# Kernel optimization log

Hardware: AMD Instinct MI355X
Metric: run time of the kernel (lower is better)

Reference implementation:

```python
import jax, jax.numpy as jnp
import numpy as np

B, S, H, NH, PF, L = 2, 2048, 1024, 16, 4096, 6
HD = H // NH
EPS = 1e-5


def setup_inputs() -> dict:
    key = jax.random.key(0)
    ks = jax.random.split(key, 12)
    s = lambda k, shp, fan: jax.random.normal(k, shp, jnp.float32) * (1.0 / np.sqrt(fan))
    return {
        "input_tensor": jax.random.normal(ks[0], (B, S, H), jnp.float32),
        "pos_emb": s(ks[1], (S, H), H),
        "Wq": s(ks[2], (L, H, H), H), "bq": jnp.zeros((L, H), jnp.float32),
        "Wk": s(ks[3], (L, H, H), H), "bk": jnp.zeros((L, H), jnp.float32),
        "Wv": s(ks[4], (L, H, H), H), "bv": jnp.zeros((L, H), jnp.float32),
        "Wo": s(ks[5], (L, H, H), H), "bo": jnp.zeros((L, H), jnp.float32),
        "ln_g": jnp.ones((L, H), jnp.float32), "ln_b": jnp.zeros((L, H), jnp.float32),
        "W1": s(ks[6], (L, H, PF), H), "b1": jnp.zeros((L, PF), jnp.float32),
        "W2": s(ks[7], (L, PF, H), PF), "b2": jnp.zeros((L, H), jnp.float32),
    }


def _layernorm(x, g, b):
    mu = jnp.mean(x, axis=-1, keepdims=True)
    var = jnp.mean(jnp.square(x - mu), axis=-1, keepdims=True)
    return (x - mu) * jax.lax.rsqrt(var + EPS) * g + b


def _encoder(input_tensor, pos_emb, params):
    # pos embed: same positions for every batch row
    src = input_tensor * jnp.sqrt(jnp.float32(H)) + pos_emb[None, :, :]

    def layer(src, p):
        Wq, bq, Wk, bk, Wv, bv, Wo, bo, g, b, W1, b1, W2, b2 = p
        q = (src @ Wq + bq).reshape(B, S, NH, HD)
        k = (src @ Wk + bk).reshape(B, S, NH, HD)
        v = (src @ Wv + bv).reshape(B, S, NH, HD)
        # scores [B, NH, S, S]
        energy = jnp.einsum("bqhd,bkhd->bhqk", q, k) / jnp.sqrt(jnp.float32(HD))
        attn = jax.nn.softmax(energy, axis=-1)
        ctx = jnp.einsum("bhqk,bkhd->bqhd", attn, v).reshape(B, S, H)
        attn_out = ctx @ Wo + bo
        src = _layernorm(src + attn_out, g, b)
        ffn = jax.nn.relu(src @ W1 + b1) @ W2 + b2
        src = _layernorm(src + ffn, g, b)  # same LayerNorm reused, as in source
        return src, None

    src, _ = jax.lax.scan(layer, src, params)
    return src


def reference(input_tensor, pos_emb, Wq, bq, Wk, bk, Wv, bv, Wo, bo, ln_g, ln_b, W1, b1, W2, b2):
    params = (Wq, bq, Wk, bk, Wv, bv, Wo, bo, ln_g, ln_b, W1, b1, W2, b2)
    return _encoder(input_tensor, pos_emb, params)
```

## Files before the change

### kernel.cpp

```cpp
#include <hip/hip_runtime.h>
#include <cstdint>

constexpr int Bc = 2, Sc = 2048, Hc = 1024, NHc = 16, HDc = 64, PFc = 4096, Lc = 6;
constexpr float EPSc = 1e-5f;
constexpr float QSC = 0.18033688011112042f;

using f32x4  = __attribute__((ext_vector_type(4))) float;
using bf16x8 = __attribute__((ext_vector_type(8))) __bf16;
using bf16x4 = __attribute__((ext_vector_type(4))) __bf16;
using u32x4  = __attribute__((ext_vector_type(4))) unsigned;

#if __has_builtin(__builtin_amdgcn_exp2f)
#define EXP2(x) __builtin_amdgcn_exp2f(x)
#else
#define EXP2(x) exp2f(x)
#endif

__device__ __forceinline__ f32x4 mfma16(bf16x8 a, bf16x8 b, f32x4 c) {
    return __builtin_amdgcn_mfma_f32_16x16x32_bf16(a, b, c, 0, 0, 0);
}

__device__ __forceinline__ void gload_lds16(const void* g, void* l) {
    __builtin_amdgcn_global_load_lds(
        (__attribute__((address_space(1))) void*)(uintptr_t)g,
        (__attribute__((address_space(3))) void*)(uint32_t)(uintptr_t)l,
        16, 0, 0);
}

struct HL { __bf16 h, l; };
__device__ __forceinline__ HL split2(float v) {
    HL r;
    r.h = (__bf16)v;
    r.l = (__bf16)(v - (float)r.h);
    return r;
}

__device__ __forceinline__ unsigned bfbits(__bf16 x) {
    return (unsigned)__builtin_bit_cast(unsigned short, x);
}
__device__ __forceinline__ unsigned packbf(float a, float b) {
    return bfbits((__bf16)a) | (bfbits((__bf16)b) << 16);
}

__device__ __forceinline__ int xcd_swz(int bid, int nwg) {
    return (bid & 7) * (nwg >> 3) + (bid >> 3);
}

__global__ __launch_bounds__(256) void wconv_kernel(
    const float* __restrict__ in, __bf16* __restrict__ out, int K, int N)
{
    __shared__ float tile[64][65];
    const int t = threadIdx.x;
    const size_t lstride = (size_t)K * N;
    const float* ip = in + (size_t)blockIdx.z * lstride;
    __bf16* op = out + (size_t)blockIdx.z * lstride;
    const int n0 = blockIdx.x * 64, k0 = blockIdx.y * 64;
    #pragma unroll
    for (int c = 0; c < 4; ++c) {
        int idx = c * 256 + t;
        int row = idx >> 4;
        int c4  = idx & 15;
        float4 v = *(const float4*)(ip + (size_t)(k0 + row) * N + n0 + c4 * 4);
        tile[row][c4 * 4 + 0] = v.x; tile[row][c4 * 4 + 1] = v.y;
        tile[row][c4 * 4 + 2] = v.z; tile[row][c4 * 4 + 3] = v.w;
    }
    __syncthreads();
    #pragma unroll
    for (int c = 0; c < 4; ++c) {
        int idx = c * 256 + t;
        int n  = idx >> 4;
        int k4 = idx & 15;
        bf16x4 hh = { (__bf16)tile[k4 * 4 + 0][n], (__bf16)tile[k4 * 4 + 1][n],
                      (__bf16)tile[k4 * 4 + 2][n], (__bf16)tile[k4 * 4 + 3][n] };
        *(bf16x4*)(op + (size_t)(n0 + n) * K + k0 + k4 * 4) = hh;
    }
}

__global__ __launch_bounds__(256) void wconv2_kernel(
    const float* __restrict__ in, __bf16* __restrict__ outh,
    __bf16* __restrict__ outl, int K, int N)
{
    __shared__ float tile[64][65];
    const int t = threadIdx.x;
    const int n0 = blockIdx.x * 64, k0 = blockIdx.y * 64;
    #pragma unroll
    for (int c = 0; c < 4; ++c) {
        int idx = c * 256 + t;
        int row = idx >> 4;
        int c4  = idx & 15;
        float4 v = *(const float4*)(in + (size_t)(k0 + row) * N + n0 + c4 * 4);
        tile[row][c4 * 4 + 0] = v.x; tile[row][c4 * 4 + 1] = v.y;
        tile[row][c4 * 4 + 2] = v.z; tile[row][c4 * 4 + 3] = v.w;
    }
    __syncthreads();
    #pragma unroll
    for (int c = 0; c < 4; ++c) {
        int idx = c * 256 + t;
        int n  = idx >> 4;
        int k4 = idx & 15;
        HL e0 = split2(tile[k4 * 4 + 0][n]);
        HL e1 = split2(tile[k4 * 4 + 1][n]);
        HL e2 = split2(tile[k4 * 4 + 2][n]);
        HL e3 = split2(tile[k4 * 4 + 3][n]);
        bf16x4 hh = { e0.h, e1.h, e2.h, e3.h };
        bf16x4 ll = { e0.l, e1.l, e2.l, e3.l };
        *(bf16x4*)(outh + (size_t)(n0 + n) * K + k0 + k4 * 4) = hh;
        *(bf16x4*)(outl + (size_t)(n0 + n) * K + k0 + k4 * 4) = ll;
    }
}

__global__ __launch_bounds__(256) void embed_kernel(
    const float* __restrict__ in, const float* __restrict__ pos,
    float* __restrict__ sf, __bf16* __restrict__ sh, __bf16* __restrict__ sl)
{
    const int n4 = (Bc * Sc * Hc) / 4;
    const int pmask = (Sc * Hc / 4) - 1;
    for (int i = blockIdx.x * 256 + threadIdx.x; i < n4; i += gridDim.x * 256) {
        float4 a = ((const float4*)in)[i];
        float4 p = ((const float4*)pos)[i & pmask];
        float4 r;
        r.x = a.x * 32.f + p.x; r.y = a.y * 32.f + p.y;
        r.z = a.z * 32.f + p.z; r.w = a.w * 32.f + p.w;
        ((float4*)sf)[i] = r;
        HL e0 = split2(r.x), e1 = split2(r.y), e2 = split2(r.z), e3 = split2(r.w);
        bf16x4 hh = { e0.h, e1.h, e2.h, e3.h };
        bf16x4 ll = { e0.l, e1.l, e2.l, e3.l };
        ((bf16x4*)sh)[i] = hh;
        ((bf16x4*)sl)[i] = ll;
    }
}

template<int BM, int OUTMODE, bool RELU>
__global__ __launch_bounds__(256) void gemm_bt_kernel(
    const __bf16* __restrict__ A, const __bf16* __restrict__ Wt,
    const float* __restrict__ bias, void* __restrict__ out,
    int M, int N, int K)
{
    constexpr int MI = BM / 32;
    __shared__ alignas(16) __bf16 Alds[2][BM * 64];
    __shared__ alignas(16) __bf16 Blds[2][128 * 64];

    const int tid = threadIdx.x, lane = tid & 63, wave = tid >> 6;
    const int lr = lane & 15, lg = lane >> 4;
    const int nbx = gridDim.x;
    const int swz = xcd_swz(blockIdx.y * nbx + blockIdx.x, nbx * gridDim.y);
    const int m0 = (swz / nbx) * BM, n0 = (swz % nbx) * 128;
    const int wm = (wave >> 1) * (BM / 2), wn = (wave & 1) * 64;

    f32x4 acc[MI][4] = {};

    auto stage = [&](int k0, int buf) {
        #pragma unroll
        for (int c = 0; c < BM / 32; ++c) {
            int li = c * 256 + tid;
            int row = li >> 3;
            int lcb = ((li & 7) << 4) ^ ((row & 7) << 4);
            gload_lds16(A + (size_t)(m0 + row) * K + k0 + (lcb >> 1),
                        (char*)Alds[buf] + (size_t)(c * 256 + wave * 64) * 16);
        }
        #pragma unroll
        for (int c = 0; c < 4; ++c) {
            int li = c * 256 + tid;
            int row = li >> 3;
            int lcb = ((li & 7) << 4) ^ ((row & 7) << 4);
            gload_lds16(Wt + (size_t)(n0 + row) * K + k0 + (lcb >> 1),
                        (char*)Blds[buf] + (size_t)(c * 256 + wave * 64) * 16);
        }
    };

    stage(0, 0);
    __syncthreads();
    int cur = 0;

    for (int k0 = 0; k0 < K; k0 += 64) {
        if (k0 + 64 < K) stage(k0 + 64, cur ^ 1);

        bf16x8 af[2][MI], bfr[2][4];
        #pragma unroll
        for (int ks = 0; ks < 2; ++ks) {
            #pragma unroll
            for (int i = 0; i < MI; ++i) {
                int ra = wm + i * 16 + lr;
                int pa = (ks * 64 + lg * 16) ^ ((ra & 7) << 4);
                af[ks][i] = *(const bf16x8*)((const char*)Alds[cur] + ra * 128 + pa);
            }
            #pragma unroll
            for (int i = 0; i < 4; ++i) {
                int rb = wn + i * 16 + lr;
                int pb = (ks * 64 + lg * 16) ^ ((rb & 7) << 4);
                bfr[ks][i] = *(const bf16x8*)((const char*)Blds[cur] + rb * 128 + pb);
            }
        }
        #pragma unroll
        for (int ks = 0; ks < 2; ++ks)
            #pragma unroll
            for (int mi = 0; mi < MI; ++mi)
                #pragma unroll
                for (int ni = 0; ni < 4; ++ni)
                    acc[mi][ni] = mfma16(af[ks][mi], bfr[ks][ni], acc[mi][ni]);

        __syncthreads();
        cur ^= 1;
    }

    #pragma unroll
    for (int ni = 0; ni < 4; ++ni) {
        int col = n0 + wn + ni * 16 + lr;
        float bv = bias[col];
        #pragma unroll
        for (int mi = 0; mi < MI; ++mi) {
            int rowb = m0 + wm + mi * 16 + lg * 4;
            #pragma unroll
            for (int r = 0; r < 4; ++r) {
                float v = acc[mi][ni][r] + bv;
                if (RELU) v = fmaxf(v, 0.f);
                size_t idx = (size_t)(rowb + r) * N + col;
                if constexpr (OUTMODE == 0) ((float*)out)[idx] = v;
                else                        ((__bf16*)out)[idx] = (__bf16)v;
            }
        }
    }
}

struct QKVBT {
    const __bf16 *wq, *wk, *wv;
    const float *bq, *bk, *bv;
    __bf16 *q, *k, *v;
};

__global__ __launch_bounds__(256) void qkv_bt_kernel(
    const __bf16* __restrict__ A, QKVBT a)
{
    constexpr int N = Hc, K = Hc;
    __shared__ alignas(16) __bf16 Alds[2][128 * 64];
    __shared__ alignas(16) __bf16 Blds[2][128 * 64];

    const int tid = threadIdx.x, lane = tid & 63, wave = tid >> 6;
    const int lr = lane & 15, lg = lane >> 4;
    const int nbx = gridDim.x;
    const int swz = xcd_swz(blockIdx.y * nbx + blockIdx.x, nbx * gridDim.y);
    const int gx = swz % nbx;
    const int widx = gx >> 3;
    const int n0 = (gx & 7) * 128;
    const int m0 = (swz / nbx) * 128;
    const int wm = (wave >> 1) * 64, wn = (wave & 1) * 64;

    const __bf16* Wt  = (widx == 0) ? a.wq : (widx == 1) ? a.wk : a.wv;
    const float* bias = (widx == 0) ? a.bq : (widx == 1) ? a.bk : a.bv;

    f32x4 acc[4][4] = {};

    auto stage = [&](int k0, int buf) {
        #pragma unroll
        for (int c = 0; c < 4; ++c) {
            int li = c * 256 + tid;
            int row = li >> 3;
            int lcb = ((li & 7) << 4) ^ ((row & 7) << 4);
            gload_lds16(A + (size_t)(m0 + row) * K + k0 + (lcb >> 1),
                        (char*)Alds[buf] + (size_t)(c * 256 + wave * 64) * 16);
            gload_lds16(Wt + (size_t)(n0 + row) * K + k0 + (lcb >> 1),
                        (char*)Blds[buf] + (size_t)(c * 256 + wave * 64) * 16);
        }
    };

    stage(0, 0);
    __syncthreads();
    int cur = 0;

    for (int k0 = 0; k0 < K; k0 += 64) {
        if (k0 + 64 < K) stage(k0 + 64, cur ^ 1);

        bf16x8 af[2][4], bfr[2][4];
        #pragma unroll
        for (int ks = 0; ks < 2; ++ks) {
            #pragma unroll
            for (int i = 0; i < 4; ++i) {
                int ra = wm + i * 16 + lr;
                int pa = (ks * 64 + lg * 16) ^ ((ra & 7) << 4);
                af[ks][i] = *(const bf16x8*)((const char*)Alds[cur] + ra * 128 + pa);
                int rb = wn + i * 16 + lr;
                int pb = (ks * 64 + lg * 16) ^ ((rb & 7) << 4);
                bfr[ks][i] = *(const bf16x8*)((const char*)Blds[cur] + rb * 128 + pb);
            }
        }
        #pragma unroll
        for (int ks = 0; ks < 2; ++ks)
            #pragma unroll
            for (int mi = 0; mi < 4; ++mi)
                #pragma unroll
                for (int ni = 0; ni < 4; ++ni)
                    acc[mi][ni] = mfma16(af[ks][mi], bfr[ks][ni], acc[mi][ni]);

        __syncthreads();
        cur ^= 1;
    }

    __bf16* outp = (widx == 0) ? a.q : (widx == 1) ? a.k : a.v;
    const float osc = (widx == 0) ? QSC : 1.f;
    #pragma unroll
    for (int ni = 0; ni < 4; ++ni) {
        int col = n0 + wn + ni * 16 + lr;
        float bv = bias[col];
        int hh = col >> 6, d = col & 63;
        #pragma unroll
        for (int mi = 0; mi < 4; ++mi) {
            int rowb = m0 + wm + mi * 16 + lg * 4;
            #pragma unroll
            for (int r = 0; r < 4; ++r) {
                int row = rowb + r;
                int bb = row >> 11, s = row & (Sc - 1);
                outp[((size_t)(bb * NHc + hh) * Sc + s) * HDc + d] =
                    (__bf16)((acc[mi][ni][r] + bv) * osc);
            }
        }
    }
}

struct QKV0S {
    const __bf16 *wqh, *wql, *wkh, *wkl, *wv;
    const float *bq, *bk, *bv;
    __bf16 *qh, *ql, *kh, *kl, *vv;
};

__global__ __launch_bounds__(256) void qkv0s_kernel(
    const __bf16* __restrict__ Ahi, const __bf16* __restrict__ Alo, QKV0S a)
{
    constexpr int N = Hc, K = Hc;
    __shared__ alignas(16) __bf16 AldsH[128 * 64];
    __shared__ alignas(16) __bf16 AldsL[128 * 64];
    __shared__ alignas(16) __bf16 BldsH[128 * 64];
    __shared__ alignas(16) __bf16 BldsL[128 * 64];

    const int tid = threadIdx.x, lane = tid & 63, wave = tid >> 6;
    const int lr = lane & 15, lg = lane >> 4;
    const int nbx = gridDim.x;
    const int swz = xcd_swz(blockIdx.y * nbx + blockIdx.x, nbx * gridDim.y);
    const int gx = swz % nbx;
    const int widx = gx >> 3;
    const int n0 = (gx & 7) * 128;
    const int m0 = (swz / nbx) * 128;
    const int wm = (wave >> 1) * 64, wn = (wave & 1) * 64;
    const bool SPLIT = (widx < 2);

    const __bf16* Bh = (widx == 0) ? a.wqh : (widx == 1) ? a.wkh : a.wv;
    const __bf16* Bl = (widx == 0) ? a.wql : a.wkl;
    const float* bias = (widx == 0) ? a.bq : (widx == 1) ? a.bk : a.bv;

    f32x4 acc[4][4] = {};

    for (int k0 = 0; k0 < K; k0 += 64) {
        #pragma unroll
        for (int c = 0; c < 4; ++c) {
            int li = c * 256 + tid;
            int row = li >> 3;
            int lcb = ((li & 7) << 4) ^ ((row & 7) << 4);
            size_t aoff = (size_t)(m0 + row) * K + k0 + (lcb >> 1);
            size_t boff = (size_t)(n0 + row) * K + k0 + (lcb >> 1);
            size_t loff = (size_t)(c * 256 + wave * 64) * 16;
            gload_lds16(Ahi + aoff, (char*)AldsH + loff);
            gload_lds16(Bh + boff, (char*)BldsH + loff);
            if (SPLIT) {
                gload_lds16(Alo + aoff, (char*)AldsL + loff);
                gload_lds16(Bl + boff, (char*)BldsL + loff);
            }
        }
        __syncthreads();

        bf16x8 ah[2][4], al[2][4], bh[2][4], bl[2][4];
        #pragma unroll
        for (int ks = 0; ks < 2; ++ks) {
            #pragma unroll
            for (int i = 0; i < 4; ++i) {
                int ra = wm + i * 16 + lr;
                int pa = (ks * 64 + lg * 16) ^ ((ra & 7) << 4);
                ah[ks][i] = *(const bf16x8*)((const char*)AldsH + ra * 128 + pa);
                int rb = wn + i * 16 + lr;
                int pb = (ks * 64 + lg * 16) ^ ((rb & 7) << 4);
                bh[ks][i] = *(const bf16x8*)((const char*)BldsH + rb * 128 + pb);
                if (SPLIT) {
                    al[ks][i] = *(const bf16x8*)((const char*)AldsL + ra * 128 + pa);
                    bl[ks][i] = *(const bf16x8*)((const char*)BldsL + rb * 128 + pb);
                }
            }
        }
        #pragma unroll
        for (int ks = 0; ks < 2; ++ks)
            #pragma unroll
            for (int mi = 0; mi < 4; ++mi)
                #pragma unroll
                for (int ni = 0; ni < 4; ++ni) {
                    acc[mi][ni] = mfma16(ah[ks][mi], bh[ks][ni], acc[mi][ni]);
                    if (SPLIT) {
                        acc[mi][ni] = mfma16(al[ks][mi], bh[ks][ni], acc[mi][ni]);
                        acc[mi][ni] = mfma16(ah[ks][mi], bl[ks][ni], acc[mi][ni]);
                    }
                }
        __syncthreads();
    }

    __bf16* outh = (widx == 0) ? a.qh : (widx == 1) ? a.kh : a.vv;
    __bf16* outl = (widx == 0) ? a.ql : a.kl;
    const float osc = (widx == 0) ? QSC : 1.f;
    #pragma unroll
    for (int ni = 0; ni < 4; ++ni) {
        int col = n0 + wn + ni * 16 + lr;
        float bv = bias[col];
        int hh = col >> 6, d = col & 63;
        #pragma unroll
        for (int mi = 0; mi < 4; ++mi) {
            int rowb = m0 + wm + mi * 16 + lg * 4;
            #pragma unroll
            for (int r = 0; r < 4; ++r) {
                int row = rowb + r;
                int bb = row >> 11, s = row & (Sc - 1);
                size_t idx = ((size_t)(bb * NHc + hh) * Sc + s) * HDc + d;
                float v = (acc[mi][ni][r] + bv) * osc;
                if (SPLIT) {
                    HL e = split2(v);
                    outh[idx] = e.h;
                    outl[idx] = e.l;
                } else {
                    outh[idx] = (__bf16)v;
                }
            }
        }
    }
}

template<int QKSPLIT>
__global__ __launch_bounds__(256) void attn_kernel(
    const __bf16* __restrict__ Qh, const __bf16* __restrict__ Ql,
    const __bf16* __restrict__ Kh, const __bf16* __restrict__ Kl,
    const __bf16* __restrict__ V, __bf16* __restrict__ O)
{
    __shared__ alignas(16) __bf16 Ksh[2][64 * 64];
    __shared__ alignas(16) __bf16 Klo[QKSPLIT ? 2 : 1][QKSPLIT ? 64 * 64 : 8];
    __shared__ alignas(16) __bf16 VT[2][64 * 64];

    const int tid = threadIdx.x;
    const int lane = tid & 63, wave = tid >> 6;
    const int lr = lane & 15, lg = lane >> 4;
    const int h = blockIdx.y, b = blockIdx.z;
    const int q0 = blockIdx.x * 128 + wave * 32;

    const size_t headoff = ((size_t)b * NHc + h) * Sc * HDc;
    const __bf16* Qb  = Qh + headoff;
    const __bf16* Kb  = Kh + headoff;
    const __bf16* Klb = QKSPLIT ? (Kl + headoff) : nullptr;
    const __bf16* Vb  = V + headoff;

    const size_t qrowA = (size_t)(q0 + lr) * HDc;
    const size_t qrowB = qrowA + 16 * HDc;
    bf16x8 qfA0 = *(const bf16x8*)(Qb + qrowA + lg * 8);
    bf16x8 qfA1 = *(const bf16x8*)(Qb + qrowA + 32 + lg * 8);
    bf16x8 qfB0 = *(const bf16x8*)(Qb + qrowB + lg * 8);
    bf16x8 qfB1 = *(const bf16x8*)(Qb + qrowB + 32 + lg * 8);
    bf16x8 qlA0, qlA1, qlB0, qlB1;
    if constexpr (QKSPLIT) {
        const __bf16* Qlb = Ql + headoff;
        qlA0 = *(const bf16x8*)(Qlb + qrowA + lg * 8);
        qlA1 = *(const bf16x8*)(Qlb + qrowA + 32 + lg * 8);
        qlB0 = *(const bf16x8*)(Qlb + qrowB + lg * 8);
        qlB1 = *(const bf16x8*)(Qlb + qrowB + 32 + lg * 8);
    }

    const int kp = tid & 31, dblk = tid >> 5;
    const int sp = (kp & 0x11) | ((kp & 0x06) << 1) | ((kp & 0x08) >> 2);

    auto stageK = [&](int kt, int buf) {
        #pragma unroll
        for (int c = 0; c < 2; ++c) {
            int li  = c * 256 + tid;
            int row = li >> 3;
            int lcb = ((li & 7) << 4) ^ ((row & 7) << 4);
            size_t goff = (size_t)(kt * 64 + row) * HDc + (lcb >> 1);
            size_t loff = (size_t)(c * 256 + wave * 64) * 16;
            gload_lds16(Kb + goff, (char*)Ksh[buf] + loff);
            if constexpr (QKSPLIT)
                gload_lds16(Klb + goff, (char*)Klo[buf] + loff);
        }
    };
    auto loadV = [&](int kt, bf16x8& va, bf16x8& vb2) {
        const __bf16* vs = Vb + (size_t)(kt * 64 + 2 * kp) * HDc + dblk * 8;
        va  = *(const bf16x8*)vs;
        vb2 = *(const bf16x8*)(vs + HDc);
    };
    auto writeVT = [&](int buf, bf16x8 va, bf16x8 vb2) {
        #pragma unroll
        for (int j = 0; j < 8; ++j) {
            int d = dblk * 8 + j;
            unsigned u = bfbits(va[j]) | (bfbits(vb2[j]) << 16);
            int byte = d * 128 + ((sp * 4) ^ ((d & 7) << 4));
            *(unsigned*)((char*)VT[buf] + byte) = u;
        }
    };

    f32x4 oA[4] = {}, oB[4] = {};
    float mA = -1e30f, mB = -1e30f, lsA = 0.f, lsB = 0.f;

    stageK(0, 0);
    {
        bf16x8 va, vb2;
        loadV(0, va, vb2);
        writeVT(0, va, vb2);
    }
    __syncthreads();

    int cur = 0;
    for (int kt = 0; kt < Sc / 64; ++kt) {
        const int nb = cur ^ 1;
        const bool pf = (kt + 1 < Sc / 64);
        bf16x8 va, vb2;
        if (pf) {
            stageK(kt + 1, nb);
            loadV(kt + 1, va, vb2);
        }

        const char* Kc = (const char*)Ksh[cur];
        const char* Klc = (const char*)Klo[QKSPLIT ? cur : 0];
        f32x4 sA[4], sB[4];
        #pragma unroll
        for (int kg = 0; kg < 4; ++kg) {
            int ra = kg * 16 + lr;
            int pa0 = (lg * 16) ^ ((ra & 7) << 4);
            int pa1 = (64 + lg * 16) ^ ((ra & 7) << 4);
            bf16x8 kf0 = *(const bf16x8*)(Kc + ra * 128 + pa0);
            bf16x8 kf1 = *(const bf16x8*)(Kc + ra * 128 + pa1);
            f32x4 tA = {}, tB = {};
            tA = mfma16(kf0, qfA0, tA);
            tA = mfma16(kf1, qfA1, tA);
            tB = mfma16(kf0, qfB0, tB);
            tB = mfma16(kf1, qfB1, tB);
            if constexpr (QKSPLIT) {
                bf16x8 kg0 = *(const bf16x8*)(Klc + ra * 128 + pa0);
                bf16x8 kg1 = *(const bf16x8*)(Klc + ra * 128 + pa1);
                tA = mfma16(kg0, qfA0, tA);
                tA = mfma16(kg1, qfA1, tA);
                tA = mfma16(kf0, qlA0, tA);
                tA = mfma16(kf1, qlA1, tA);
                tB = mfma16(kg0, qfB0, tB);
                tB = mfma16(kg1, qfB1, tB);
                tB = mfma16(kf0, qlB0, tB);
                tB = mfma16(kf1, qlB1, tB);
            }
            sA[kg] = tA;
            sB[kg] = tB;
        }

        float mtA = -1e30f, mtB = -1e30f;
        #pragma unroll
        for (int kg = 0; kg < 4; ++kg)
            #pragma unroll
            for (int r = 0; r < 4; ++r) {
                mtA = fmaxf(mtA, sA[kg][r]);
                mtB = fmaxf(mtB, sB[kg][r]);
            }
        mtA = fmaxf(mtA, __shfl_xor(mtA, 16));
        mtA = fmaxf(mtA, __shfl_xor(mtA, 32));
        mtB = fmaxf(mtB, __shfl_xor(mtB, 16));
        mtB = fmaxf(mtB, __shfl_xor(mtB, 32));
        if (!__all(mtA <= mA)) {
            float mnew = fmaxf(mA, mtA);
            float fac = EXP2(mA - mnew);
            mA = mnew;
            lsA *= fac;
            #pragma unroll
            for (int r = 0; r < 4; ++r) {
                float fr = __shfl(fac, (lg << 4) | (lg * 4 + r));
                #pragma unroll
                for (int nd = 0; nd < 4; ++nd) oA[nd][r] *= fr;
            }
        }
        if (!__all(mtB <= mB)) {
            float mnew = fmaxf(mB, mtB);
            float fac = EXP2(mB - mnew);
            mB = mnew;
            lsB *= fac;
            #pragma unroll
            for (int r = 0; r < 4; ++r) {
                float fr = __shfl(fac, (lg << 4) | (lg * 4 + r));
                #pragma unroll
                for (int nd = 0; nd < 4; ++nd) oB[nd][r] *= fr;
            }
        }
        float psA = 0.f, psB = 0.f;
        #pragma unroll
        for (int kg = 0; kg < 4; ++kg)
            #pragma unroll
            for (int r = 0; r < 4; ++r) {
                float pA = EXP2(sA[kg][r] - mA);
                float pB = EXP2(sB[kg][r] - mB);
                psA += pA;
                psB += pB;
                sA[kg][r] = pA;
                sB[kg][r] = pB;
            }
        psA += __shfl_xor(psA, 16);
        psA += __shfl_xor(psA, 32);
        psB += __shfl_xor(psB, 16);
        psB += __shfl_xor(psB, 32);
        lsA += psA;
        lsB += psB;

        #pragma unroll
        for (int kh2 = 0; kh2 < 2; ++kh2) {
            u32x4 pkA, pkB;
            pkA[0] = packbf(sA[2 * kh2][0],     sA[2 * kh2][1]);
            pkA[1] = packbf(sA[2 * kh2][2],     sA[2 * kh2][3]);
            pkA[2] = packbf(sA[2 * kh2 + 1][0], sA[2 * kh2 + 1][1]);
            pkA[3] = packbf(sA[2 * kh2 + 1][2], sA[2 * kh2 + 1][3]);
            pkB[0] = packbf(sB[2 * kh2][0],     sB[2 * kh2][1]);
            pkB[1] = packbf(sB[2 * kh2][2],     sB[2 * kh2][3]);
            pkB[2] = packbf(sB[2 * kh2 + 1][0], sB[2 * kh2 + 1][1]);
            pkB[3] = packbf(sB[2 * kh2 + 1][2], sB[2 * kh2 + 1][3]);
            bf16x8 pafA = __builtin_bit_cast(bf16x8, pkA);
            bf16x8 pafB = __builtin_bit_cast(bf16x8, pkB);
            #pragma unroll
            for (int nd = 0; nd < 4; ++nd) {
                int d = nd * 16 + lr;
                int byte = d * 128 + ((64 * kh2 + 16 * lg) ^ ((d & 7) << 4));
                bf16x8 vbf = *(const bf16x8*)((const char*)VT[cur] + byte);
                oA[nd] = mfma16(pafA, vbf, oA[nd]);
                oB[nd] = mfma16(pafB, vbf, oB[nd]);
            }
        }

        if (pf) writeVT(nb, va, vb2);
        __syncthreads();
        cur = nb;
    }

    #pragma unroll
    for (int r = 0; r < 4; ++r) {
        float lvA = __shfl(lsA, (lg << 4) | (lg * 4 + r));
        float lvB = __shfl(lsB, (lg << 4) | (lg * 4 + r));
        float invA = 1.f / lvA;
        float invB = 1.f / lvB;
        size_t orowA = ((size_t)b * Sc + q0 + lg * 4 + r) * Hc + h * HDc;
        size_t orowB = orowA + (size_t)16 * Hc;
        #pragma unroll
        for (int nd = 0; nd < 4; ++nd) {
            O[orowA + nd * 16 + lr] = (__bf16)(oA[nd][r] * invA);
            O[orowB + nd * 16 + lr] = (__bf16)(oB[nd][r] * invB);
        }
    }
}

__global__ __launch_bounds__(256) void ln_kernel(
    const float* __restrict__ xr, const __bf16* __restrict__ y,
    const float* __restrict__ g, const float* __restrict__ beta,
    float* __restrict__ of, __bf16* __restrict__ oh)
{
    __shared__ float red[2][4];
    const int row = blockIdx.x, t = threadIdx.x;
    const int lane = t & 63, wave = t >> 6;
    const int idx = row * 256 + t;
    float4 a = ((const float4*)xr)[idx];
    bf16x4 cb = ((const bf16x4*)y)[idx];
    float4 v;
    v.x = a.x + (float)cb[0]; v.y = a.y + (float)cb[1];
    v.z = a.z + (float)cb[2]; v.w = a.w + (float)cb[3];
    float s1 = v.x + v.y + v.z + v.w;
    float s2 = v.x * v.x + v.y * v.y + v.z * v.z + v.w * v.w;
    #pragma unroll
    for (int off = 1; off < 64; off <<= 1) {
        s1 += __shfl_xor(s1, off);
        s2 += __shfl_xor(s2, off);
    }
    if (lane == 0) { red[0][wave] = s1; red[1][wave] = s2; }
    __syncthreads();
    s1 = red[0][0] + red[0][1] + red[0][2] + red[0][3];
    s2 = red[1][0] + red[1][1] + red[1][2] + red[1][3];
    const float mu   = s1 * (1.f / Hc);
    const float var  = s2 * (1.f / Hc) - mu * mu;
    const float rstd = rsqrtf(var + EPSc);
    float4 gg = ((const float4*)g)[t];
    float4 bb = ((const float4*)beta)[t];
    float4 r;
    r.x = (v.x - mu) * rstd * gg.x + bb.x;
    r.y = (v.y - mu) * rstd * gg.y + bb.y;
    r.z = (v.z - mu) * rstd * gg.z + bb.z;
    r.w = (v.w - mu) * rstd * gg.w + bb.w;
    ((float4*)of)[idx] = r;
    bf16x4 hh = { (__bf16)r.x, (__bf16)r.y, (__bf16)r.z, (__bf16)r.w };
    ((bf16x4*)oh)[idx] = hh;
}

extern "C" void kernel_launch(void* const* d_in, const int* in_sizes, int n_in,
                              void* d_out, int out_size, void* d_ws, size_t ws_size,
                              hipStream_t stream)
{
    const float* inp = (const float*)d_in[0];
    const float* pos = (const float*)d_in[1];
    const float* Wq  = (const float*)d_in[2];
    const float* bq  = (const float*)d_in[3];
    const float* Wk  = (const float*)d_in[4];
    const float* bk  = (const float*)d_in[5];
    const float* Wv  = (const float*)d_in[6];
    const float* bv  = (const float*)d_in[7];
    const float* Wo  = (const float*)d_in[8];
    const float* bo  = (const float*)d_in[9];
    const float* lng = (const float*)d_in[10];
    const float* lnb = (const float*)d_in[11];
    const float* W1  = (const float*)d_in[12];
    const float* b1  = (const float*)d_in[13];
    const float* W2  = (const float*)d_in[14];
    const float* b2  = (const float*)d_in[15];

    char* ws = (char*)d_ws;
    const size_t MB = 1u << 20;
    float*  src_f = (float*)(ws);
    __bf16* src_h = (__bf16*)(ws + 16 * MB);
    __bf16* src_l = (__bf16*)(ws + 24 * MB);
    __bf16* qh    = (__bf16*)(ws + 32 * MB);
    __bf16* kh    = (__bf16*)(ws + 40 * MB);
    __bf16* vv    = (__bf16*)(ws + 48 * MB);
    __bf16* ctx   = (__bf16*)(ws + 56 * MB);
    __bf16* ql    = (__bf16*)(ws + 64 * MB);
    __bf16* kl    = (__bf16*)(ws + 72 * MB);
    __bf16* tmpb  = (__bf16*)(ws + 80 * MB);
    __bf16* wq0h  = (__bf16*)(ws + 80 * MB);
    __bf16* wq0l  = (__bf16*)(ws + 82 * MB);
    __bf16* wk0h  = (__bf16*)(ws + 84 * MB);
    __bf16* wk0l  = (__bf16*)(ws + 86 * MB);
    __bf16* h1    = (__bf16*)(ws + 32 * MB);
    __bf16* wqT   = (__bf16*)(ws + 96 * MB);
    __bf16* wkT   = (__bf16*)(ws + 108 * MB);
    __bf16* wvT   = (__bf16*)(ws + 120 * MB);
    __bf16* woT   = (__bf16*)(ws + 132 * MB);
    __bf16* w1T   = (__bf16*)(ws + 144 * MB);
    __bf16* w2T   = (__bf16*)(ws + 192 * MB);

    const int M = Bc * Sc;

    wconv_kernel<<<dim3(16, 16, 6), 256, 0, stream>>>(Wq, wqT, Hc, Hc);
    wconv_kernel<<<dim3(16, 16, 6), 256, 0, stream>>>(Wk, wkT, Hc, Hc);
    wconv_kernel<<<dim3(16, 16, 6), 256, 0, stream>>>(Wv, wvT, Hc, Hc);
    wconv_kernel<<<dim3(16, 16, 6), 256, 0, stream>>>(Wo, woT, Hc, Hc);
    wconv_kernel<<<dim3(64, 16, 6), 256, 0, stream>>>(W1, w1T, Hc, PFc);
    wconv_kernel<<<dim3(16, 64, 6), 256, 0, stream>>>(W2, w2T, PFc, Hc);
    wconv2_kernel<<<dim3(16, 16), 256, 0, stream>>>(Wq, wq0h, wq0l, Hc, Hc);
    wconv2_kernel<<<dim3(16, 16), 256, 0, stream>>>(Wk, wk0h, wk0l, Hc, Hc);

    embed_kernel<<<2048, 256, 0, stream>>>(inp, pos, src_f, src_h, src_l);

    for (int l = 0; l < Lc; ++l) {
        const size_t wHH = (size_t)l * Hc * Hc;
        const size_t wH  = (size_t)l * Hc;
        if (l == 0) {
            QKV0S qa = { wq0h, wq0l, wk0h, wk0l, wvT, bq, bk, bv,
                         qh, ql, kh, kl, vv };
            qkv0s_kernel<<<dim3(24, 32), 256, 0, stream>>>(src_h, src_l, qa);
            attn_kernel<1><<<dim3(16, 16, 2), 256, 0, stream>>>(qh, ql, kh, kl, vv, ctx);
        } else {
            QKVBT qa = { wqT + wHH, wkT + wHH, wvT + wHH, bq + wH, bk + wH, bv + wH,
                         qh, kh, vv };
            qkv_bt_kernel<<<dim3(24, 32), 256, 0, stream>>>(src_h, qa);
            attn_kernel<0><<<dim3(16, 16, 2), 256, 0, stream>>>(qh, nullptr, kh, nullptr, vv, ctx);
        }
        gemm_bt_kernel<64, 1, false><<<dim3(8, 64), 256, 0, stream>>>(
            ctx, woT + wHH, bo + wH, tmpb, M, Hc, Hc);
        ln_kernel<<<M, 256, 0, stream>>>(src_f, tmpb, lng + wH, lnb + wH, src_f, src_h);
        gemm_bt_kernel<128, 1, true><<<dim3(32, 32), 256, 0, stream>>>(
            src_h, w1T + (size_t)l * Hc * PFc, b1 + (size_t)l * PFc, h1, M, PFc, Hc);
        gemm_bt_kernel<64, 1, false><<<dim3(8, 64), 256, 0, stream>>>(
            h1, w2T + (size_t)l * PFc * Hc, b2 + wH, tmpb, M, Hc, PFc);
        float* dst = (l == Lc - 1) ? (float*)d_out : src_f;
        ln_kernel<<<M, 256, 0, stream>>>(src_f, tmpb, lng + wH, lnb + wH, dst, src_h);
    }
}
```

Measured before the change: 1.608 ms.

## Process 128-key tiles per barrier in attention and defer softmax rescaling

The attention kernel for layers 1-5 now stages two 64-key sub-tiles of K and V per double-buffer step, which halves the number of block-wide barriers and global-load rounds. It also raises wave priority around the MFMA sections with s_setprio, and it skips the online-softmax rescale unless the new row max exceeds the running max by more than 8 (in log2 units). The larger tiles double LDS use and the registers held for prefetched V. Letting the running max lag can raise exp values by up to 2^8, which is meant to stay safe in fp32 and bf16 while avoiding frequent rescale work.

```diff
diff --git a/kernel.cpp b/kernel.cpp
--- a/kernel.cpp
+++ b/kernel.cpp
@@ -427,15 +427,16 @@
     }
 }
 
-template<int QKSPLIT>
+template<int QKSPLIT, int NH2>
 __global__ __launch_bounds__(256) void attn_kernel(
     const __bf16* __restrict__ Qh, const __bf16* __restrict__ Ql,
     const __bf16* __restrict__ Kh, const __bf16* __restrict__ Kl,
     const __bf16* __restrict__ V, __bf16* __restrict__ O)
 {
-    __shared__ alignas(16) __bf16 Ksh[2][64 * 64];
+    constexpr int KVB = 64 * NH2;
+    __shared__ alignas(16) __bf16 Ksh[2][KVB * 64];
     __shared__ alignas(16) __bf16 Klo[QKSPLIT ? 2 : 1][QKSPLIT ? 64 * 64 : 8];
-    __shared__ alignas(16) __bf16 VT[2][64 * 64];
+    __shared__ alignas(16) __bf16 VT[2][NH2][64 * 64];
 
     const int tid = threadIdx.x;
     const int lane = tid & 63, wave = tid >> 6;
@@ -469,29 +470,29 @@
 
     auto stageK = [&](int kt, int buf) {
         #pragma unroll
-        for (int c = 0; c < 2; ++c) {
+        for (int c = 0; c < 2 * NH2; ++c) {
             int li  = c * 256 + tid;
             int row = li >> 3;
             int lcb = ((li & 7) << 4) ^ ((row & 7) << 4);
-            size_t goff = (size_t)(kt * 64 + row) * HDc + (lcb >> 1);
+            size_t goff = (size_t)(kt * KVB + row) * HDc + (lcb >> 1);
             size_t loff = (size_t)(c * 256 + wave * 64) * 16;
             gload_lds16(Kb + goff, (char*)Ksh[buf] + loff);
             if constexpr (QKSPLIT)
                 gload_lds16(Klb + goff, (char*)Klo[buf] + loff);
         }
     };
-    auto loadV = [&](int kt, bf16x8& va, bf16x8& vb2) {
-        const __bf16* vs = Vb + (size_t)(kt * 64 + 2 * kp) * HDc + dblk * 8;
+    auto loadV = [&](int kt, int half, bf16x8& va, bf16x8& vb2) {
+        const __bf16* vs = Vb + (size_t)(kt * KVB + half * 64 + 2 * kp) * HDc + dblk * 8;
         va  = *(const bf16x8*)vs;
         vb2 = *(const bf16x8*)(vs + HDc);
     };
-    auto writeVT = [&](int buf, bf16x8 va, bf16x8 vb2) {
+    auto writeVT = [&](int buf, int half, bf16x8 va, bf16x8 vb2) {
         #pragma unroll
         for (int j = 0; j < 8; ++j) {
             int d = dblk * 8 + j;
             unsigned u = bfbits(va[j]) | (bfbits(vb2[j]) << 16);
             int byte = d * 128 + ((sp * 4) ^ ((d & 7) << 4));
-            *(unsigned*)((char*)VT[buf] + byte) = u;
+            *(unsigned*)((char*)VT[buf][half] + byte) = u;
         }
     };
 
@@ -501,131 +502,147 @@
     stageK(0, 0);
     {
         bf16x8 va, vb2;
-        loadV(0, va, vb2);
-        writeVT(0, va, vb2);
+        #pragma unroll
+        for (int hf = 0; hf < NH2; ++hf) {
+            loadV(0, hf, va, vb2);
+            writeVT(0, hf, va, vb2);
+        }
     }
     __syncthreads();
 
+    const int NT = Sc / KVB;
     int cur = 0;
-    for (int kt = 0; kt < Sc / 64; ++kt) {
+    for (int kt = 0; kt < NT; ++kt) {
         const int nb = cur ^ 1;
-        const bool pf = (kt + 1 < Sc / 64);
-        bf16x8 va, vb2;
+        const bool pf = (kt + 1 < NT);
+        bf16x8 va[NH2], vb2[NH2];
         if (pf) {
             stageK(kt + 1, nb);
-            loadV(kt + 1, va, vb2);
-        }
-
-        const char* Kc = (const char*)Ksh[cur];
+            #pragma unroll
+            for (int hf = 0; hf < NH2; ++hf) loadV(kt + 1, hf, va[hf], vb2[hf]);
+        }
+
+        const char* Kc  = (const char*)Ksh[cur];
         const char* Klc = (const char*)Klo[QKSPLIT ? cur : 0];
-        f32x4 sA[4], sB[4];
-        #pragma unroll
-        for (int kg = 0; kg < 4; ++kg) {
-            int ra = kg * 16 + lr;
-            int pa0 = (lg * 16) ^ ((ra & 7) << 4);
-            int pa1 = (64 + lg * 16) ^ ((ra & 7) << 4);
-            bf16x8 kf0 = *(const bf16x8*)(Kc + ra * 128 + pa0);
-            bf16x8 kf1 = *(const bf16x8*)(Kc + ra * 128 + pa1);
-            f32x4 tA = {}, tB = {};
-            tA = mfma16(kf0, qfA0, tA);
-            tA = mfma16(kf1, qfA1, tA);
-            tB = mfma16(kf0, qfB0, tB);
-            tB = mfma16(kf1, qfB1, tB);
-            if constexpr (QKSPLIT) {
-                bf16x8 kg0 = *(const bf16x8*)(Klc + ra * 128 + pa0);
-                bf16x8 kg1 = *(const bf16x8*)(Klc + ra * 128 + pa1);
-                tA = mfma16(kg0, qfA0, tA);
-                tA = mfma16(kg1, qfA1, tA);
-                tA = mfma16(kf0, qlA0, tA);
-                tA = mfma16(kf1, qlA1, tA);
-                tB = mfma16(kg0, qfB0, tB);
-                tB = mfma16(kg1, qfB1, tB);
-                tB = mfma16(kf0, qlB0, tB);
-                tB = mfma16(kf1, qlB1, tB);
-            }
-            sA[kg] = tA;
-            sB[kg] = tB;
-        }
-
-        float mtA = -1e30f, mtB = -1e30f;
-        #pragma unroll
-        for (int kg = 0; kg < 4; ++kg)
-            #pragma unroll
-            for (int r = 0; r < 4; ++r) {
-                mtA = fmaxf(mtA, sA[kg][r]);
-                mtB = fmaxf(mtB, sB[kg][r]);
-            }
-        mtA = fmaxf(mtA, __shfl_xor(mtA, 16));
-        mtA = fmaxf(mtA, __shfl_xor(mtA, 32));
-        mtB = fmaxf(mtB, __shfl_xor(mtB, 16));
-        mtB = fmaxf(mtB, __shfl_xor(mtB, 32));
-        if (!__all(mtA <= mA)) {
-            float mnew = fmaxf(mA, mtA);
-            float fac = EXP2(mA - mnew);
-            mA = mnew;
-            lsA *= fac;
-            #pragma unroll
-            for (int r = 0; r < 4; ++r) {
-                float fr = __shfl(fac, (lg << 4) | (lg * 4 + r));
+
+        #pragma unroll
+        for (int half = 0; half < NH2; ++half) {
+            f32x4 sA[4], sB[4];
+            __builtin_amdgcn_s_setprio(1);
+            #pragma unroll
+            for (int kg = 0; kg < 4; ++kg) {
+                int ra = half * 64 + kg * 16 + lr;
+                int pa0 = (lg * 16) ^ ((ra & 7) << 4);
+                int pa1 = (64 + lg * 16) ^ ((ra & 7) << 4);
+                bf16x8 kf0 = *(const bf16x8*)(Kc + ra * 128 + pa0);
+                bf16x8 kf1 = *(const bf16x8*)(Kc + ra * 128 + pa1);
+                f32x4 tA = {}, tB = {};
+                tA = mfma16(kf0, qfA0, tA);
+                tA = mfma16(kf1, qfA1, tA);
+                tB = mfma16(kf0, qfB0, tB);
+                tB = mfma16(kf1, qfB1, tB);
+                if constexpr (QKSPLIT) {
+                    bf16x8 kg0 = *(const bf16x8*)(Klc + ra * 128 + pa0);
+                    bf16x8 kg1 = *(const bf16x8*)(Klc + ra * 128 + pa1);
+                    tA = mfma16(kg0, qfA0, tA);
+                    tA = mfma16(kg1, qfA1, tA);
+                    tA = mfma16(kf0, qlA0, tA);
+                    tA = mfma16(kf1, qlA1, tA);
+                    tB = mfma16(kg0, qfB0, tB);
+                    tB = mfma16(kg1, qfB1, tB);
+                    tB = mfma16(kf0, qlB0, tB);
+                    tB = mfma16(kf1, qlB1, tB);
+                }
+                sA[kg] = tA;
+                sB[kg] = tB;
+            }
+            __builtin_amdgcn_s_setprio(0);
+
+            float mtA = -1e30f, mtB = -1e30f;
+            #pragma unroll
+            for (int kg = 0; kg < 4; ++kg)
                 #pragma unroll
-                for (int nd = 0; nd < 4; ++nd) oA[nd][r] *= fr;
-            }
-        }
-        if (!__all(mtB <= mB)) {
-            float mnew = fmaxf(mB, mtB);
-            float fac = EXP2(mB - mnew);
-            mB = mnew;
-            lsB *= fac;
-            #pragma unroll
-            for (int r = 0; r < 4; ++r) {
-                float fr = __shfl(fac, (lg << 4) | (lg * 4 + r));
+                for (int r = 0; r < 4; ++r) {
+                    mtA = fmaxf(mtA, sA[kg][r]);
+                    mtB = fmaxf(mtB, sB[kg][r]);
+                }
+            mtA = fmaxf(mtA, __shfl_xor(mtA, 16));
+            mtA = fmaxf(mtA, __shfl_xor(mtA, 32));
+            mtB = fmaxf(mtB, __shfl_xor(mtB, 16));
+            mtB = fmaxf(mtB, __shfl_xor(mtB, 32));
+            if (!__all(mtA <= mA + 8.f)) {
+                float mnew = fmaxf(mA, mtA);
+                float fac = EXP2(mA - mnew);
+                mA = mnew;
+                lsA *= fac;
                 #pragma unroll
-                for (int nd = 0; nd < 4; ++nd) oB[nd][r] *= fr;
-            }
-        }
-        float psA = 0.f, psB = 0.f;
-        #pragma unroll
-        for (int kg = 0; kg < 4; ++kg)
-            #pragma unroll
-            for (int r = 0; r < 4; ++r) {
-                float pA = EXP2(sA[kg][r] - mA);
-                float pB = EXP2(sB[kg][r] - mB);
-                psA += pA;
-                psB += pB;
-                sA[kg][r] = pA;
-                sB[kg][r] = pB;
-            }
-        psA += __shfl_xor(psA, 16);
-        psA += __shfl_xor(psA, 32);
-        psB += __shfl_xor(psB, 16);
-        psB += __shfl_xor(psB, 32);
-        lsA += psA;
-        lsB += psB;
-
-        #pragma unroll
-        for (int kh2 = 0; kh2 < 2; ++kh2) {
-            u32x4 pkA, pkB;
-            pkA[0] = packbf(sA[2 * kh2][0],     sA[2 * kh2][1]);
-            pkA[1] = packbf(sA[2 * kh2][2],     sA[2 * kh2][3]);
-            pkA[2] = packbf(sA[2 * kh2 + 1][0], sA[2 * kh2 + 1][1]);
-            pkA[3] = packbf(sA[2 * kh2 + 1][2], sA[2 * kh2 + 1][3]);
-            pkB[0] = packbf(sB[2 * kh2][0],     sB[2 * kh2][1]);
-            pkB[1] = packbf(sB[2 * kh2][2],     sB[2 * kh2][3]);
-            pkB[2] = packbf(sB[2 * kh2 + 1][0], sB[2 * kh2 + 1][1]);
-            pkB[3] = packbf(sB[2 * kh2 + 1][2], sB[2 * kh2 + 1][3]);
-            bf16x8 pafA = __builtin_bit_cast(bf16x8, pkA);
-            bf16x8 pafB = __builtin_bit_cast(bf16x8, pkB);
-            #pragma unroll
-            for (int nd = 0; nd < 4; ++nd) {
-                int d = nd * 16 + lr;
-                int byte = d * 128 + ((64 * kh2 + 16 * lg) ^ ((d & 7) << 4));
-                bf16x8 vbf = *(const bf16x8*)((const char*)VT[cur] + byte);
-                oA[nd] = mfma16(pafA, vbf, oA[nd]);
-                oB[nd] = mfma16(pafB, vbf, oB[nd]);
-            }
-        }
-
-        if (pf) writeVT(nb, va, vb2);
+                for (int r = 0; r < 4; ++r) {
+                    float fr = __shfl(fac, (lg << 4) | (lg * 4 + r));
+                    #pragma unroll
+                    for (int nd = 0; nd < 4; ++nd) oA[nd][r] *= fr;
+                }
+            }
+            if (!__all(mtB <= mB + 8.f)) {
+                float mnew = fmaxf(mB, mtB);
+                float fac = EXP2(mB - mnew);
+                mB = mnew;
+                lsB *= fac;
+                #pragma unroll
+                for (int r = 0; r < 4; ++r) {
+                    float fr = __shfl(fac, (lg << 4) | (lg * 4 + r));
+                    #pragma unroll
+                    for (int nd = 0; nd < 4; ++nd) oB[nd][r] *= fr;
+                }
+            }
+            float psA = 0.f, psB = 0.f;
+            #pragma unroll
+            for (int kg = 0; kg < 4; ++kg)
+                #pragma unroll
+                for (int r = 0; r < 4; ++r) {
+                    float pA = EXP2(sA[kg][r] - mA);
+                    float pB = EXP2(sB[kg][r] - mB);
+                    psA += pA;
+                    psB += pB;
+                    sA[kg][r] = pA;
+                    sB[kg][r] = pB;
+                }
+            psA += __shfl_xor(psA, 16);
+            psA += __shfl_xor(psA, 32);
+            psB += __shfl_xor(psB, 16);
+            psB += __shfl_xor(psB, 32);
+            lsA += psA;
+            lsB += psB;
+
+            #pragma unroll
+            for (int kh2 = 0; kh2 < 2; ++kh2) {
+                u32x4 pkA, pkB;
+                pkA[0] = packbf(sA[2 * kh2][0],     sA[2 * kh2][1]);
+                pkA[1] = packbf(sA[2 * kh2][2],     sA[2 * kh2][3]);
+                pkA[2] = packbf(sA[2 * kh2 + 1][0], sA[2 * kh2 + 1][1]);
+                pkA[3] = packbf(sA[2 * kh2 + 1][2], sA[2 * kh2 + 1][3]);
+                pkB[0] = packbf(sB[2 * kh2][0],     sB[2 * kh2][1]);
+                pkB[1] = packbf(sB[2 * kh2][2],     sB[2 * kh2][3]);
+                pkB[2] = packbf(sB[2 * kh2 + 1][0], sB[2 * kh2 + 1][1]);
+                pkB[3] = packbf(sB[2 * kh2 + 1][2], sB[2 * kh2 + 1][3]);
+                bf16x8 pafA = __builtin_bit_cast(bf16x8, pkA);
+                bf16x8 pafB = __builtin_bit_cast(bf16x8, pkB);
+                __builtin_amdgcn_s_setprio(1);
+                #pragma unroll
+                for (int nd = 0; nd < 4; ++nd) {
+                    int d = nd * 16 + lr;
+                    int byte = d * 128 + ((64 * kh2 + 16 * lg) ^ ((d & 7) << 4));
+                    bf16x8 vbf = *(const bf16x8*)((const char*)VT[cur][half] + byte);
+                    oA[nd] = mfma16(pafA, vbf, oA[nd]);
+                    oB[nd] = mfma16(pafB, vbf, oB[nd]);
+                }
+                __builtin_amdgcn_s_setprio(0);
+            }
+        }
+
+        if (pf) {
+            #pragma unroll
+            for (int hf = 0; hf < NH2; ++hf) writeVT(nb, hf, va[hf], vb2[hf]);
+        }
         __syncthreads();
         cur = nb;
     }
@@ -751,12 +768,12 @@
             QKV0S qa = { wq0h, wq0l, wk0h, wk0l, wvT, bq, bk, bv,
                          qh, ql, kh, kl, vv };
             qkv0s_kernel<<<dim3(24, 32), 256, 0, stream>>>(src_h, src_l, qa);
-            attn_kernel<1><<<dim3(16, 16, 2), 256, 0, stream>>>(qh, ql, kh, kl, vv, ctx);
+            attn_kernel<1, 1><<<dim3(16, 16, 2), 256, 0, stream>>>(qh, ql, kh, kl, vv, ctx);
         } else {
             QKVBT qa = { wqT + wHH, wkT + wHH, wvT + wHH, bq + wH, bk + wH, bv + wH,
                          qh, kh, vv };
             qkv_bt_kernel<<<dim3(24, 32), 256, 0, stream>>>(src_h, qa);
-            attn_kernel<0><<<dim3(16, 16, 2), 256, 0, stream>>>(qh, nullptr, kh, nullptr, vv, ctx);
+            attn_kernel<0, 2><<<dim3(16, 16, 2), 256, 0, stream>>>(qh, nullptr, kh, nullptr, vv, ctx);
         }
         gemm_bt_kernel<64, 1, false><<<dim3(8, 64), 256, 0, stream>>>(
             ctx, woT + wHH, bo + wH, tmpb, M, Hc, Hc);
```

Result: no change. 1.586 ms (-1.4%).
